# Performance work log

Hardware: AMD Instinct MI355X
Metric: run time of the kernel (lower is better)

## Reference

```python
import jax, jax.numpy as jnp
import numpy as np

B, S, D = 4, 1024, 1024
H = 16
DH = D // H           # 64
ROT = 64              # rotary_emb_dim (full head dim)
NEG_INF = -10000.0
ROPE_BASE = 10000.0


def _rope_tables(seqlen, rot_dim, dtype=jnp.float32):
    inv_freq = 1.0 / (ROPE_BASE ** (jnp.arange(0, rot_dim, 2, dtype=jnp.float32) / rot_dim))
    t = jnp.arange(seqlen, dtype=jnp.float32)
    freqs = jnp.einsum('s,f->sf', t, inv_freq)  # (S, rot_dim//2)
    return jnp.cos(freqs).astype(dtype), jnp.sin(freqs).astype(dtype)


def _apply_rotary(x, cos, sin):
    # x: (B, S, H, DH); GPT-NeoX (non-interleaved) rotary over first ROT dims
    half = ROT // 2
    x_rot, x_pass = x[..., :ROT], x[..., ROT:]
    x1, x2 = x_rot[..., :half], x_rot[..., half:]
    c = cos[None, :, None, :]
    s = sin[None, :, None, :]
    rot = jnp.concatenate([x1 * c - x2 * s, x2 * c + x1 * s], axis=-1)
    return jnp.concatenate([rot, x_pass], axis=-1) if x_pass.shape[-1] else rot


def setup_inputs() -> dict:
    key = jax.random.key(0)
    ks = jax.random.split(key, 5)
    sc_in = 1.0 / np.sqrt(D)
    return {
        'x': jax.random.normal(ks[0], (B, S, D), jnp.float32),
        'Wqkv': jax.random.normal(ks[1], (3 * D, D), jnp.float32) * sc_in,
        'bqkv': jax.random.normal(ks[2], (3 * D,), jnp.float32) * 0.01,
        'Wout': jax.random.normal(ks[3], (D, D), jnp.float32) * sc_in,
        'bout': jax.random.normal(ks[4], (D,), jnp.float32) * 0.01,
    }


def reference(x, Wqkv, bqkv, Wout, bout):
    # QKV projection: (B,S,D) -> (B,S,3,H,DH)
    qkv = (jnp.einsum('bsd,ed->bse', x, Wqkv) + bqkv).reshape(B, S, 3, H, DH)
    q, k, v = qkv[:, :, 0], qkv[:, :, 1], qkv[:, :, 2]
    cos, sin = _rope_tables(S, ROT, q.dtype)
    q = _apply_rotary(q, cos, sin)
    k = _apply_rotary(k, cos, sin)
    scale = 1.0 / np.sqrt(DH)
    scores = jnp.einsum('bthd,bshd->bhts', q, k * scale)  # (B,H,S,S)
    causal_mask = jnp.triu(jnp.full((S, S), NEG_INF, dtype=scores.dtype), 1)
    scores = scores + causal_mask
    attn = jax.nn.softmax(scores, axis=-1)
    out = jnp.einsum('bhts,bshd->bthd', attn, v).reshape(B, S, D)
    return jnp.einsum('bsd,ed->bse', out, Wout) + bout
```

## Files before the change

### kernel.cpp

```cpp
#include <hip/hip_runtime.h>

#define B_ 4
#define S_ 1024
#define D_ 1024
#define H_ 16
#define DH_ 64

typedef unsigned short u16;
typedef __attribute__((ext_vector_type(8))) short bf16x8;
typedef __attribute__((ext_vector_type(4))) float f32x4;

__device__ __forceinline__ float bf2f(u16 h){
  union { unsigned u; float f; } x; x.u = ((unsigned)h) << 16; return x.f;
}
__device__ __forceinline__ u16 f2bf(float f){
  union { float f; unsigned u; } x; x.f = f;
  unsigned u = x.u;
  return (u16)((u + 0x7fffu + ((u >> 16) & 1u)) >> 16);
}

__device__ __forceinline__ void gload16(const u16* g, u16* l){
  __builtin_amdgcn_global_load_lds(
      (const __attribute__((address_space(1))) unsigned int*)g,
      (__attribute__((address_space(3))) unsigned int*)l, 16, 0, 0);
}

__global__ __launch_bounds__(256) void cast3(
    const float* __restrict__ a, u16* __restrict__ oa, int na,
    const float* __restrict__ b, u16* __restrict__ ob, int nb,
    const float* __restrict__ c, u16* __restrict__ oc){
  int i = (blockIdx.x * 256 + threadIdx.x) * 4;
  const float* src; u16* dst;
  if (i < na){ src = a + i; dst = oa + i; }
  else if (i < na + nb){ src = b + (i - na); dst = ob + (i - na); }
  else { src = c + (i - na - nb); dst = oc + (i - na - nb); }
  float4 v = *(const float4*)src;
  union { u16 s[4]; uint2 u; } o;
  o.s[0] = f2bf(v.x); o.s[1] = f2bf(v.y); o.s[2] = f2bf(v.z); o.s[3] = f2bf(v.w);
  *(uint2*)dst = o.u;
}

__global__ __launch_bounds__(256) void rope_tab(float2* __restrict__ tab){
  int idx = blockIdx.x * 256 + threadIdx.x;
  int s = idx >> 5, i = idx & 31;
  float invf = powf(10000.0f, -(float)i * (1.0f / 32.0f));
  float sn, cs;
  sincosf((float)s * invf, &sn, &cs);
  tab[idx] = make_float2(cs, sn);
}

__global__ __launch_bounds__(512, 2) void gemm_qkv8(const u16* __restrict__ A,
    const u16* __restrict__ Bm, const float* __restrict__ bias,
    const float2* __restrict__ tab,
    u16* __restrict__ qb, u16* __restrict__ kb, u16* __restrict__ vtb){
  __shared__ u16 As_[2][2][128*64];
  __shared__ u16 Bs_[2][2][128*64];
  const int K = 1024;
  const int tid = threadIdx.x;
  const int lane = tid & 63, wid = tid >> 6;
  const int wr = wid >> 2, wc = wid & 3;
  const int lo = lane & 15, g = lane >> 4;

  const int bid = blockIdx.x;
  const int swz = (bid & 7) * 24 + (bid >> 3);
  const int bx = swz & 15, by = swz >> 4;
  const int m0 = bx * 256, n0 = by * 256;

  f32x4 acc[8][4];
  #pragma unroll
  for (int i = 0; i < 8; ++i)
    #pragma unroll
    for (int j = 0; j < 4; ++j) acc[i][j] = (f32x4){0.f, 0.f, 0.f, 0.f};

  auto stage_p0 = [&](int b, int kt){
    const u16* ga = A + (size_t)m0 * K + kt * 64;
    const u16* gb = Bm + (size_t)n0 * K + kt * 64;
    {
      int c = tid;
      int r = c >> 3;
      int colbs = ((c & 7) * 16) ^ ((r & 7) << 4);
      int src = r * K + (colbs >> 1);
      gload16(ga + src,         &As_[b][0][c * 8]);
      gload16(ga + 128*K + src, &As_[b][1][c * 8]);
      gload16(gb + src,         &Bs_[b][0][c * 8]);
      gload16(gb + 128*K + src, &Bs_[b][1][c * 8]);
    }
    {
      int c = tid + 512;
      int r = c >> 3;
      int colbs = ((c & 7) * 16) ^ ((r & 7) << 4);
      int src = r * K + (colbs >> 1);
      gload16(gb + src,         &Bs_[b][0][c * 8]);
      gload16(gb + 128*K + src, &Bs_[b][1][c * 8]);
    }
  };
  auto stage_p1 = [&](int b, int kt){
    const u16* ga = A + (size_t)m0 * K + kt * 64;
    int c = tid + 512;
    int r = c >> 3;
    int colbs = ((c & 7) * 16) ^ ((r & 7) << 4);
    int src = r * K + (colbs >> 1);
    gload16(ga + src,         &As_[b][0][c * 8]);
    gload16(ga + 128*K + src, &As_[b][1][c * 8]);
  };

  auto rdA = [&](int b, int qm, int fm, int ks) -> bf16x8 {
    int row = qm*64 + fm*16 + lo;
    int byte = row*128 + ((ks*64 + g*16) ^ ((lo & 7) << 4));
    return *(const bf16x8*)(&As_[b][wr][byte >> 1]);
  };
  auto rdB = [&](int b, int fn, int ks) -> bf16x8 {
    int row = (wc & 1)*64 + fn*16 + lo;
    int byte = row*128 + ((ks*64 + g*16) ^ ((lo & 7) << 4));
    return *(const bf16x8*)(&Bs_[b][wc >> 1][byte >> 1]);
  };

  auto ktile = [&](int b, int stage_t){
    bf16x8 a[8], bq[8];
    #pragma unroll
    for (int fm = 0; fm < 4; ++fm)
      #pragma unroll
      for (int ks = 0; ks < 2; ++ks) a[fm*2+ks] = rdA(b, 0, fm, ks);
    #pragma unroll
    for (int fn = 0; fn < 4; ++fn)
      #pragma unroll
      for (int ks = 0; ks < 2; ++ks) bq[fn*2+ks] = rdB(b, fn, ks);
    __builtin_amdgcn_s_setprio(1);
    #pragma unroll
    for (int fm = 0; fm < 4; ++fm)
      #pragma unroll
      for (int fn = 0; fn < 2; ++fn)
        #pragma unroll
        for (int ks = 0; ks < 2; ++ks)
          acc[fm][fn] = __builtin_amdgcn_mfma_f32_16x16x32_bf16(a[fm*2+ks], bq[fn*2+ks], acc[fm][fn], 0, 0, 0);
    __builtin_amdgcn_s_setprio(0);
    asm volatile("s_waitcnt lgkmcnt(0)" ::: "memory");
    __builtin_amdgcn_sched_barrier(0);
    __builtin_amdgcn_s_barrier();
    __builtin_amdgcn_sched_barrier(0);
    if (stage_t >= 0) stage_p0(b, stage_t);
    __builtin_amdgcn_s_setprio(1);
    #pragma unroll
    for (int fm = 0; fm < 4; ++fm)
      #pragma unroll
      for (int fn = 0; fn < 2; ++fn)
        #pragma unroll
        for (int ks = 0; ks < 2; ++ks)
          acc[fm][2+fn] = __builtin_amdgcn_mfma_f32_16x16x32_bf16(a[fm*2+ks], bq[(2+fn)*2+ks], acc[fm][2+fn], 0, 0, 0);
    __builtin_amdgcn_s_setprio(0);
    #pragma unroll
    for (int fm = 0; fm < 4; ++fm)
      #pragma unroll
      for (int ks = 0; ks < 2; ++ks) a[fm*2+ks] = rdA(b, 1, fm, ks);
    __builtin_amdgcn_s_setprio(1);
    #pragma unroll
    for (int fm = 0; fm < 4; ++fm)
      #pragma unroll
      for (int fn = 0; fn < 2; ++fn)
        #pragma unroll
        for (int ks = 0; ks < 2; ++ks)
          acc[4+fm][fn] = __builtin_amdgcn_mfma_f32_16x16x32_bf16(a[fm*2+ks], bq[fn*2+ks], acc[4+fm][fn], 0, 0, 0);
    __builtin_amdgcn_s_setprio(0);
    asm volatile("s_waitcnt lgkmcnt(0)" ::: "memory");
    __builtin_amdgcn_sched_barrier(0);
    __builtin_amdgcn_s_barrier();
    __builtin_amdgcn_sched_barrier(0);
    if (stage_t >= 0) stage_p1(b, stage_t);
    __builtin_amdgcn_s_setprio(1);
    #pragma unroll
    for (int fm = 0; fm < 4; ++fm)
      #pragma unroll
      for (int fn = 0; fn < 2; ++fn)
        #pragma unroll
        for (int ks = 0; ks < 2; ++ks)
          acc[4+fm][2+fn] = __builtin_amdgcn_mfma_f32_16x16x32_bf16(a[fm*2+ks], bq[(2+fn)*2+ks], acc[4+fm][2+fn], 0, 0, 0);
    __builtin_amdgcn_s_setprio(0);
  };

  stage_p0(0, 0); stage_p1(0, 0);
  stage_p0(1, 1); stage_p1(1, 1);
  for (int t = 0; t < 14; ++t){
    asm volatile("s_waitcnt vmcnt(8)" ::: "memory");
    __builtin_amdgcn_s_barrier();
    __builtin_amdgcn_sched_barrier(0);
    ktile(t & 1, t + 2);
  }
  asm volatile("s_waitcnt vmcnt(8)" ::: "memory");
  __builtin_amdgcn_s_barrier();
  __builtin_amdgcn_sched_barrier(0);
  ktile(0, -1);
  asm volatile("s_waitcnt vmcnt(0)" ::: "memory");
  __builtin_amdgcn_s_barrier();
  __builtin_amdgcn_sched_barrier(0);
  ktile(1, -1);

  const int ty = by >> 2;
  const int h  = (by & 3) * 4 + wc;
  float bv[4];
  #pragma unroll
  for (int fn = 0; fn < 4; ++fn) bv[fn] = bias[n0 + wc*64 + fn*16 + lo];

  if (ty < 2){
    u16* dst = (ty == 0) ? qb : kb;
    #pragma unroll
    for (int fm = 0; fm < 8; ++fm){
      #pragma unroll
      for (int j = 0; j < 4; ++j){
        int row = m0 + wr*128 + fm*16 + g*4 + j;
        int bb = row >> 10, s = row & 1023;
        size_t obase = (((size_t)(bb * H_ + h)) * S_ + s) * DH_;
        #pragma unroll
        for (int fn = 0; fn < 2; ++fn){
          int i = fn*16 + lo;
          float2 t2 = tab[s*32 + i];
          float v1 = acc[fm][fn][j] + bv[fn];
          float v2 = acc[fm][fn+2][j] + bv[fn+2];
          dst[obase + i]      = f2bf(v1 * t2.x - v2 * t2.y);
          dst[obase + i + 32] = f2bf(v2 * t2.x + v1 * t2.y);
        }
      }
    }
  } else {
    __syncthreads();
    u16* wbase = (wid < 4) ? ((u16*)As_ + wid * 8192)
                           : ((u16*)Bs_ + (wid - 4) * 8192);
    #pragma unroll
    for (int fm = 0; fm < 8; ++fm)
      #pragma unroll
      for (int fn = 0; fn < 4; ++fn){
        int d = fn*16 + lo;
        #pragma unroll
        for (int j = 0; j < 4; ++j){
          int sl = fm*16 + g*4 + j;
          int sx = sl ^ ((d & 7) << 4);
          wbase[d*128 + sx] = f2bf(acc[fm][fn][j] + bv[fn]);
        }
      }
    const int rowblk = m0 + wr*128;
    const int bb = rowblk >> 10;
    const int sbase = rowblk & 1023;
    #pragma unroll
    for (int pass = 0; pass < 16; ++pass){
      int d = pass*4 + g;
      int sc = lo * 8;
      int sx = sc ^ ((d & 7) << 4);
      bf16x8 v = *(const bf16x8*)(&wbase[d*128 + sx]);
      *(bf16x8*)(vtb + (((size_t)(bb * H_ + h)) * DH_ + d) * S_ + sbase + sc) = v;
    }
  }
}

template<int OUT_BF16>
__global__ __launch_bounds__(256) void gemm_bt(const u16* __restrict__ A,
    const u16* __restrict__ Bm, const float* __restrict__ bias,
    void* __restrict__ Cout, int M, int N, int K){
  __shared__ u16 As[2][128*32];
  __shared__ u16 Bs[2][128*32];
  const int tid = threadIdx.x;
  const int lane = tid & 63;
  const int w = tid >> 6;
  const int wr = w >> 1, wc = w & 1;
  const int lo = lane & 15, g = lane >> 4;
  const int m0 = blockIdx.x * 128, n0 = blockIdx.y * 128;

  f32x4 acc[4][4];
  #pragma unroll
  for (int i = 0; i < 4; ++i)
    #pragma unroll
    for (int j = 0; j < 4; ++j) acc[i][j] = (f32x4){0.f, 0.f, 0.f, 0.f};

  const int nt = K >> 5;

  auto stage = [&](int buf, int kt){
    const u16* ga = A + (size_t)m0 * K + kt * 32;
    const u16* gb = Bm + (size_t)n0 * K + kt * 32;
    #pragma unroll
    for (int it = 0; it < 2; ++it){
      int chunk = tid + it * 256;
      int row = chunk >> 2;
      int c0 = (chunk & 3) * 8;
      gload16(ga + (size_t)row * K + c0, &As[buf][chunk * 8]);
      gload16(gb + (size_t)row * K + c0, &Bs[buf][chunk * 8]);
    }
  };

  stage(0, 0);
  __syncthreads();
  int buf = 0;
  for (int kt = 0; kt < nt; ++kt){
    if (kt + 1 < nt) stage(buf ^ 1, kt + 1);
    bf16x8 af[4], bfr[4];
    #pragma unroll
    for (int mi = 0; mi < 4; ++mi)
      af[mi] = *(const bf16x8*)(&As[buf][(wr*64 + mi*16 + lo)*32 + g*8]);
    #pragma unroll
    for (int ni = 0; ni < 4; ++ni)
      bfr[ni] = *(const bf16x8*)(&Bs[buf][(wc*64 + ni*16 + lo)*32 + g*8]);
    #pragma unroll
    for (int mi = 0; mi < 4; ++mi)
      #pragma unroll
      for (int ni = 0; ni < 4; ++ni)
        acc[mi][ni] = __builtin_amdgcn_mfma_f32_16x16x32_bf16(af[mi], bfr[ni], acc[mi][ni], 0, 0, 0);
    __syncthreads();
    buf ^= 1;
  }

  #pragma unroll
  for (int mi = 0; mi < 4; ++mi){
    int row = m0 + wr*64 + mi*16 + g*4;
    #pragma unroll
    for (int ni = 0; ni < 4; ++ni){
      int col = n0 + wc*64 + ni*16 + lo;
      float bvs = bias[col];
      #pragma unroll
      for (int j = 0; j < 4; ++j){
        float v = acc[mi][ni][j] + bvs;
        if (OUT_BF16) ((u16*)Cout)[(size_t)(row + j) * N + col] = f2bf(v);
        else          ((float*)Cout)[(size_t)(row + j) * N + col] = v;
      }
    }
  }
}

__global__ __launch_bounds__(256) void attn_fwd(const u16* __restrict__ qb,
    const u16* __restrict__ kb, const u16* __restrict__ vtb,
    u16* __restrict__ ctx){
  const int bh = blockIdx.x;
  const int qt = 15 - blockIdx.y;
  const int b = bh >> 4, h = bh & 15;
  const int tid = threadIdx.x;
  const int lane = tid & 63, w = tid >> 6;
  const int lo = lane & 15, g = lane >> 4;

  __shared__ u16 Kl[2][64*64];
  __shared__ u16 Vl[2][64*64];
  __shared__ u16 Plds[4][16][72];

  auto stage = [&](int buf, int kt){
    const u16* ksrc = kb  + ((size_t)bh * S_ + kt*64) * DH_;
    const u16* vsrc = vtb + (size_t)bh * DH_ * S_ + kt*64;
    #pragma unroll
    for (int it = 0; it < 2; ++it){
      int c = tid + it * 256;
      int row = c >> 3;
      int colbs = ((c & 7) * 16) ^ ((row & 7) << 4);
      gload16(ksrc + (size_t)row * DH_ + (colbs >> 1), &Kl[buf][c * 8]);
      gload16(vsrc + (size_t)row * S_  + (colbs >> 1), &Vl[buf][c * 8]);
    }
  };

  stage(0, 0);

  bf16x8 qf[2];
  {
    const u16* qa = qb + ((size_t)bh * S_ + qt*64 + w*16 + lo) * DH_ + g*8;
    qf[0] = *(const bf16x8*)(qa);  qf[1] = *(const bf16x8*)(qa + 32);
  }

  float m_run[4], l_run[4];
  f32x4 O[4];
  #pragma unroll
  for (int j = 0; j < 4; ++j){ m_run[j] = -1e30f; l_run[j] = 0.f; }
  #pragma unroll
  for (int c = 0; c < 4; ++c) O[c] = (f32x4){0.f,0.f,0.f,0.f};

  int buf = 0;

  auto computeTile = [&](bool diag){
    f32x4 sacc[4];
    #pragma unroll
    for (int c = 0; c < 4; ++c) sacc[c] = (f32x4){0.f,0.f,0.f,0.f};
    __builtin_amdgcn_s_setprio(1);
    #pragma unroll
    for (int cf = 0; cf < 4; ++cf){
      int r = cf*16 + lo;
      #pragma unroll
      for (int ks = 0; ks < 2; ++ks){
        int byteoff = r*128 + ((ks*64 + g*16) ^ ((lo & 7) << 4));
        bf16x8 kf = *(const bf16x8*)(&Kl[buf][byteoff >> 1]);
        sacc[cf] = __builtin_amdgcn_mfma_f32_16x16x32_bf16(qf[ks], kf, sacc[cf], 0, 0, 0);
      }
    }
    __builtin_amdgcn_s_setprio(0);
    #pragma unroll
    for (int cf = 0; cf < 4; ++cf){
      #pragma unroll
      for (int j = 0; j < 4; ++j){
        float sv = sacc[cf][j] * 0.125f;
        if (diag){
          int kj = cf*16 + lo;
          int qr = w*16 + g*4 + j;
          if (kj > qr) sv -= 10000.f;
        }
        sacc[cf][j] = sv;
      }
    }
    float rowmax[4];
    #pragma unroll
    for (int j = 0; j < 4; ++j){
      float v = fmaxf(fmaxf(sacc[0][j], sacc[1][j]), fmaxf(sacc[2][j], sacc[3][j]));
      v = fmaxf(v, __shfl_xor(v, 1));
      v = fmaxf(v, __shfl_xor(v, 2));
      v = fmaxf(v, __shfl_xor(v, 4));
      v = fmaxf(v, __shfl_xor(v, 8));
      rowmax[j] = v;
    }
    float need = fmaxf(fmaxf(rowmax[0]-m_run[0], rowmax[1]-m_run[1]),
                       fmaxf(rowmax[2]-m_run[2], rowmax[3]-m_run[3]));
    float rsum[4] = {0.f,0.f,0.f,0.f};
    if (__all(need <= 8.0f)){
      #pragma unroll
      for (int cf = 0; cf < 4; ++cf)
        #pragma unroll
        for (int j = 0; j < 4; ++j){
          float pv = __expf(sacc[cf][j] - m_run[j]);
          sacc[cf][j] = pv;
          rsum[j] += pv;
        }
      #pragma unroll
      for (int j = 0; j < 4; ++j){
        float v = rsum[j];
        v += __shfl_xor(v, 1);
        v += __shfl_xor(v, 2);
        v += __shfl_xor(v, 4);
        v += __shfl_xor(v, 8);
        l_run[j] += v;
      }
    } else {
      float alpha[4];
      #pragma unroll
      for (int j = 0; j < 4; ++j){
        float mnew = fmaxf(m_run[j], rowmax[j]);
        alpha[j] = __expf(m_run[j] - mnew);
        m_run[j] = mnew;
      }
      #pragma unroll
      for (int cf = 0; cf < 4; ++cf)
        #pragma unroll
        for (int j = 0; j < 4; ++j){
          float pv = __expf(sacc[cf][j] - m_run[j]);
          sacc[cf][j] = pv;
          rsum[j] += pv;
        }
      #pragma unroll
      for (int j = 0; j < 4; ++j){
        float v = rsum[j];
        v += __shfl_xor(v, 1);
        v += __shfl_xor(v, 2);
        v += __shfl_xor(v, 4);
        v += __shfl_xor(v, 8);
        l_run[j] = l_run[j] * alpha[j] + v;
      }
      #pragma unroll
      for (int c = 0; c < 4; ++c)
        #pragma unroll
        for (int j = 0; j < 4; ++j) O[c][j] *= alpha[j];
    }

    #pragma unroll
    for (int cf = 0; cf < 4; ++cf){
      #pragma unroll
      for (int jp = 0; jp < 2; ++jp){
        unsigned pk;
        asm("v_cvt_pk_bf16_f32 %0, %1, %2"
            : "=v"(pk) : "v"(sacc[cf][jp*2]), "v"(sacc[cf][jp*2+1]));
        Plds[w][g*4 + jp*2][cf*16 + lo]     = (u16)(pk & 0xffffu);
        Plds[w][g*4 + jp*2 + 1][cf*16 + lo] = (u16)(pk >> 16);
      }
    }

    __builtin_amdgcn_s_setprio(1);
    #pragma unroll
    for (int ks = 0; ks < 2; ++ks){
      bf16x8 pf = *(const bf16x8*)(&Plds[w][lo][ks*32 + g*8]);
      #pragma unroll
      for (int ocf = 0; ocf < 4; ++ocf){
        int r = ocf*16 + lo;
        int byteoff = r*128 + ((ks*64 + g*16) ^ ((lo & 7) << 4));
        bf16x8 vf = *(const bf16x8*)(&Vl[buf][byteoff >> 1]);
        O[ocf] = __builtin_amdgcn_mfma_f32_16x16x32_bf16(pf, vf, O[ocf], 0, 0, 0);
      }
    }
    __builtin_amdgcn_s_setprio(0);
  };

  for (int kt = 0; kt <= qt; ++kt){
    __syncthreads();
    if (kt < qt) stage(buf ^ 1, kt + 1);
    computeTile(kt == qt);
    buf ^= 1;
  }

  float inv[4];
  #pragma unroll
  for (int j = 0; j < 4; ++j) inv[j] = 1.0f / l_run[j];
  #pragma unroll
  for (int ocf = 0; ocf < 4; ++ocf){
    #pragma unroll
    for (int j = 0; j < 4; ++j){
      int d = ocf*16 + lo;
      int qi = qt*64 + w*16 + g*4 + j;
      ctx[((size_t)(b * S_ + qi)) * D_ + h * DH_ + d] = f2bf(O[ocf][j] * inv[j]);
    }
  }
}

extern "C" void kernel_launch(void* const* d_in, const int* in_sizes, int n_in,
                              void* d_out, int out_size, void* d_ws, size_t ws_size,
                              hipStream_t stream){
  (void)in_sizes; (void)n_in; (void)out_size; (void)ws_size;
  const float* x    = (const float*)d_in[0];
  const float* Wqkv = (const float*)d_in[1];
  const float* bqkv = (const float*)d_in[2];
  const float* Wout = (const float*)d_in[3];
  const float* bout = (const float*)d_in[4];
  float* out = (float*)d_out;

  char* p = (char*)d_ws;
  u16* x_bf    = (u16*)p; p += (size_t)4096*1024*2;
  u16* wqkv_bf = (u16*)p; p += (size_t)3072*1024*2;
  u16* wout_bf = (u16*)p; p += (size_t)1024*1024*2;
  u16* q_bf    = (u16*)p; p += (size_t)4096*1024*2;
  u16* k_bf    = (u16*)p; p += (size_t)4096*1024*2;
  u16* vt_bf   = (u16*)p; p += (size_t)4096*1024*2;
  u16* ctx_bf  = (u16*)p; p += (size_t)4096*1024*2;
  float2* tab  = (float2*)p; p += (size_t)1024*32*8;

  const int na = 4096*1024, nb = 3072*1024;
  cast3<<<8192, 256, 0, stream>>>(x, x_bf, na, Wqkv, wqkv_bf, nb, Wout, wout_bf);
  rope_tab<<<128, 256, 0, stream>>>(tab);

  gemm_qkv8<<<192, 512, 0, stream>>>(x_bf, wqkv_bf, bqkv, tab, q_bf, k_bf, vt_bf);

  attn_fwd<<<dim3(64, 16), 256, 0, stream>>>(q_bf, k_bf, vt_bf, ctx_bf);

  gemm_bt<0><<<dim3(32, 8), 256, 0, stream>>>(ctx_bf, wout_bf, bout, out, 4096, 1024, 1024);
}
```

Baseline: 109.3 us.

## Split GEMM tile staging into finer phases interleaved with LDS reads and MFMA

Splits the QKV GEMM k-tile prefetch into smaller pieces. A0 and the B first half are issued after the first MFMA block, the B second half after the second, and A1 after the third. B fragment reads are also split so that only the rows still needed stay resident before their buffer region is overwritten. The goal is to spread global-to-LDS traffic more evenly across the k-tile and overlap it with compute. In exchange it adds extra workgroup barriers per k-tile, and the vmcnt(8) accounting and the buffer-reuse ordering must remain correct.

Result: slower. 118.8 us (+8.7%).

```diff
diff --git a/kernel.cpp b/kernel.cpp
--- a/kernel.cpp
+++ b/kernel.cpp
@@ -72,36 +72,38 @@
     #pragma unroll
     for (int j = 0; j < 4; ++j) acc[i][j] = (f32x4){0.f, 0.f, 0.f, 0.f};
 
-  auto stage_p0 = [&](int b, int kt){
+  auto stage_A0 = [&](int b, int kt){
     const u16* ga = A + (size_t)m0 * K + kt * 64;
+    int r = tid >> 3;
+    int cc = tid & 7;
+    int colbs = (cc * 16) ^ ((r & 7) << 4);
+    int src = r * K + (colbs >> 1);
+    gload16(ga + src,         &As_[b][0][(r*8 + cc)*8]);
+    gload16(ga + 128*K + src, &As_[b][1][(r*8 + cc)*8]);
+  };
+  auto stage_A1 = [&](int b, int kt){
+    const u16* ga = A + (size_t)m0 * K + kt * 64;
+    int r = 64 + (tid >> 3);
+    int cc = tid & 7;
+    int colbs = (cc * 16) ^ ((r & 7) << 4);
+    int src = r * K + (colbs >> 1);
+    gload16(ga + src,         &As_[b][0][(r*8 + cc)*8]);
+    gload16(ga + 128*K + src, &As_[b][1][(r*8 + cc)*8]);
+  };
+  auto stage_B = [&](int b, int kt, int half){
     const u16* gb = Bm + (size_t)n0 * K + kt * 64;
-    {
-      int c = tid;
-      int r = c >> 3;
-      int colbs = ((c & 7) * 16) ^ ((r & 7) << 4);
-      int src = r * K + (colbs >> 1);
-      gload16(ga + src,         &As_[b][0][c * 8]);
-      gload16(ga + 128*K + src, &As_[b][1][c * 8]);
-      gload16(gb + src,         &Bs_[b][0][c * 8]);
-      gload16(gb + 128*K + src, &Bs_[b][1][c * 8]);
-    }
-    {
-      int c = tid + 512;
-      int r = c >> 3;
-      int colbs = ((c & 7) * 16) ^ ((r & 7) << 4);
-      int src = r * K + (colbs >> 1);
-      gload16(gb + src,         &Bs_[b][0][c * 8]);
-      gload16(gb + 128*K + src, &Bs_[b][1][c * 8]);
-    }
-  };
-  auto stage_p1 = [&](int b, int kt){
-    const u16* ga = A + (size_t)m0 * K + kt * 64;
-    int c = tid + 512;
-    int r = c >> 3;
-    int colbs = ((c & 7) * 16) ^ ((r & 7) << 4);
-    int src = r * K + (colbs >> 1);
-    gload16(ga + src,         &As_[b][0][c * 8]);
-    gload16(ga + 128*K + src, &As_[b][1][c * 8]);
+    #pragma unroll
+    for (int it = 0; it < 2; ++it){
+      int idx = tid + it * 512;
+      int panel = idx >> 9;
+      int q = idx & 511;
+      int rr = q >> 3;
+      int row = (rr & 31) + ((rr & 32) << 1) + half * 32;
+      int cc = q & 7;
+      int colbs = (cc * 16) ^ ((row & 7) << 4);
+      int src = (size_t)(panel*128 + row) * K + (colbs >> 1);
+      gload16(gb + src, &Bs_[b][panel][(row*8 + cc)*8]);
+    }
   };
 
   auto rdA = [&](int b, int qm, int fm, int ks) -> bf16x8 {
@@ -122,9 +124,12 @@
       #pragma unroll
       for (int ks = 0; ks < 2; ++ks) a[fm*2+ks] = rdA(b, 0, fm, ks);
     #pragma unroll
-    for (int fn = 0; fn < 4; ++fn)
+    for (int fn = 0; fn < 2; ++fn)
       #pragma unroll
       for (int ks = 0; ks < 2; ++ks) bq[fn*2+ks] = rdB(b, fn, ks);
+    __builtin_amdgcn_s_barrier();
+    asm volatile("s_waitcnt lgkmcnt(0)" ::: "memory");
+    __builtin_amdgcn_sched_barrier(0);
     __builtin_amdgcn_s_setprio(1);
     #pragma unroll
     for (int fm = 0; fm < 4; ++fm)
@@ -134,11 +139,15 @@
         for (int ks = 0; ks < 2; ++ks)
           acc[fm][fn] = __builtin_amdgcn_mfma_f32_16x16x32_bf16(a[fm*2+ks], bq[fn*2+ks], acc[fm][fn], 0, 0, 0);
     __builtin_amdgcn_s_setprio(0);
+    __builtin_amdgcn_s_barrier();
+    if (stage_t >= 0){ stage_A0(b, stage_t); stage_B(b, stage_t, 0); }
+    #pragma unroll
+    for (int fn = 2; fn < 4; ++fn)
+      #pragma unroll
+      for (int ks = 0; ks < 2; ++ks) bq[fn*2+ks] = rdB(b, fn, ks);
+    __builtin_amdgcn_s_barrier();
     asm volatile("s_waitcnt lgkmcnt(0)" ::: "memory");
     __builtin_amdgcn_sched_barrier(0);
-    __builtin_amdgcn_s_barrier();
-    __builtin_amdgcn_sched_barrier(0);
-    if (stage_t >= 0) stage_p0(b, stage_t);
     __builtin_amdgcn_s_setprio(1);
     #pragma unroll
     for (int fm = 0; fm < 4; ++fm)
@@ -148,10 +157,15 @@
         for (int ks = 0; ks < 2; ++ks)
           acc[fm][2+fn] = __builtin_amdgcn_mfma_f32_16x16x32_bf16(a[fm*2+ks], bq[(2+fn)*2+ks], acc[fm][2+fn], 0, 0, 0);
     __builtin_amdgcn_s_setprio(0);
+    __builtin_amdgcn_s_barrier();
+    if (stage_t >= 0) stage_B(b, stage_t, 1);
     #pragma unroll
     for (int fm = 0; fm < 4; ++fm)
       #pragma unroll
       for (int ks = 0; ks < 2; ++ks) a[fm*2+ks] = rdA(b, 1, fm, ks);
+    __builtin_amdgcn_s_barrier();
+    asm volatile("s_waitcnt lgkmcnt(0)" ::: "memory");
+    __builtin_amdgcn_sched_barrier(0);
     __builtin_amdgcn_s_setprio(1);
     #pragma unroll
     for (int fm = 0; fm < 4; ++fm)
@@ -161,11 +175,8 @@
         for (int ks = 0; ks < 2; ++ks)
           acc[4+fm][fn] = __builtin_amdgcn_mfma_f32_16x16x32_bf16(a[fm*2+ks], bq[fn*2+ks], acc[4+fm][fn], 0, 0, 0);
     __builtin_amdgcn_s_setprio(0);
-    asm volatile("s_waitcnt lgkmcnt(0)" ::: "memory");
-    __builtin_amdgcn_sched_barrier(0);
-    __builtin_amdgcn_s_barrier();
-    __builtin_amdgcn_sched_barrier(0);
-    if (stage_t >= 0) stage_p1(b, stage_t);
+    __builtin_amdgcn_s_barrier();
+    if (stage_t >= 0) stage_A1(b, stage_t);
     __builtin_amdgcn_s_setprio(1);
     #pragma unroll
     for (int fm = 0; fm < 4; ++fm)
@@ -177,8 +188,8 @@
     __builtin_amdgcn_s_setprio(0);
   };
 
-  stage_p0(0, 0); stage_p1(0, 0);
-  stage_p0(1, 1); stage_p1(1, 1);
+  stage_A0(0, 0); stage_B(0, 0, 0); stage_B(0, 0, 1); stage_A1(0, 0);
+  stage_A0(1, 1); stage_B(1, 1, 0); stage_B(1, 1, 1); stage_A1(1, 1);
   for (int t = 0; t < 14; ++t){
     asm volatile("s_waitcnt vmcnt(8)" ::: "memory");
     __builtin_amdgcn_s_barrier();
```
